# Kernel optimization log

Hardware: AMD Instinct MI355X
Metric: run time of the kernel (lower is better)

The kernel has to match this reference:

```python
import jax, jax.numpy as jnp
import numpy as np

N_POINTS = 32768
N_PRIMS = 2048
C_LIGHT = 299792458.0


def setup_inputs() -> dict:
    key = jax.random.key(0)
    k1, k2, k3, k4, k5 = jax.random.split(key, 5)
    # query points and primitive centers in a ~room-scale scene (metres)
    query_points = jax.random.normal(k1, (N_POINTS, 3), dtype=jnp.float32) * 2.0
    positions = jax.random.normal(k2, (N_PRIMS, 3), dtype=jnp.float32) * 2.0
    # diagonal anisotropic scales, kept away from zero for stability
    scales = jax.random.uniform(k3, (N_PRIMS, 3), dtype=jnp.float32, minval=0.1, maxval=1.0)
    amplitudes = jax.random.uniform(k4, (N_PRIMS,), dtype=jnp.float32, minval=0.0, maxval=1.0)
    phases = jax.random.uniform(k5, (N_PRIMS,), dtype=jnp.float32, minval=-np.pi, maxval=np.pi)
    return {
        "query_points": query_points,
        "positions": positions,
        "scales": scales,
        "amplitudes": amplitudes,
        "phases": phases,
        "frequency": 2400000000,  # 2.4 GHz
    }


def reference(query_points, positions, scales, amplitudes, phases, frequency):
    """Batched equivalent of: field = sum_p primitive_p.evaluate(query_points, frequency).

    Each complex Gaussian primitive contributes
        a_p * exp(-0.5 * (x-mu_p)^T diag(1/s_p^2) (x-mu_p)) * exp(i*(phi_p + k*|x-mu_p|))
    with wavenumber k = 2*pi*f/c. All pairwise terms are expressed as GEMMs.
    """
    f = jnp.float32(frequency)
    k_wave = jnp.float32(2.0 * np.pi) * f / jnp.float32(C_LIGHT)

    inv_var = 1.0 / (scales * scales)                      # [P,3]
    x2 = query_points * query_points                       # [N,3]
    mu2w = jnp.sum(positions * positions * inv_var, axis=1)  # [P]
    # Mahalanobis distance^2: sum_d (x_d-mu_d)^2 / s_d^2, expanded into GEMMs
    maha = (x2 @ inv_var.T
            - 2.0 * (query_points @ (positions * inv_var).T)
            + mu2w[None, :])                               # [N,P]
    maha = jnp.maximum(maha, 0.0)
    # Euclidean distance for the propagation phase
    d2 = (jnp.sum(x2, axis=1, keepdims=True)
          - 2.0 * (query_points @ positions.T)
          + jnp.sum(positions * positions, axis=1)[None, :])  # [N,P]
    r = jnp.sqrt(jnp.maximum(d2, 1e-12))

    w = amplitudes[None, :] * jnp.exp(-0.5 * maha)         # [N,P] real envelope
    ph = phases[None, :] + k_wave * r                      # [N,P] total phase
    field = jax.lax.complex(jnp.sum(w * jnp.cos(ph), axis=1),
                            jnp.sum(w * jnp.sin(ph), axis=1))  # [N] complex64
    return field
```

## Files before the change

### kernel.cpp

```cpp
#include <hip/hip_runtime.h>
#include <math.h>

#define NPOINTS 32768
#define NPRIMS  2048
#define BLK     256
#define PBLK    (NPOINTS / BLK)
#define TILE    128

__device__ __forceinline__ float read_freq(const void* p) {
    const unsigned* w = (const unsigned*)p;
    unsigned lo = w[0];
    float ff = __uint_as_float(lo);
    if (ff >= 1.0e5f && ff <= 1.0e13f) return ff;
    if (lo != 0u) return (float)lo;
    double d = *(const double*)p;
    if (d >= 1.0e5 && d <= 1.0e13) return (float)d;
    unsigned long long v = ((unsigned long long)w[1] << 32) | lo;
    return (float)v;
}

template <int NS, bool DIRECT>
__global__ __launch_bounds__(BLK) void field_kernel(
        const float* __restrict__ qp,
        const float* __restrict__ pos,
        const float* __restrict__ scl,
        const float* __restrict__ amp,
        const float* __restrict__ ph,
        const void*  __restrict__ freq_p,
        float*       __restrict__ out_or_part) {
    constexpr int PC = NPRIMS / NS;
    constexpr int NT = PC / TILE;
    __shared__ float4 sA[TILE];
    __shared__ float4 sB[TILE];

    const int n = blockIdx.x * BLK + threadIdx.x;
    const float x = qp[3*n+0], y = qp[3*n+1], z = qp[3*n+2];
    const float kr = read_freq(freq_p) / 299792458.0f;

    const int split = blockIdx.y;
    float re = 0.0f, im = 0.0f;

    const float KE     = -0.72134752044448169f;
    const float INV2PI =  0.15915494309189535f;

    for (int tile = 0; tile < NT; ++tile) {
        const int pbase = split * PC + tile * TILE;
        __syncthreads();
        if (threadIdx.x < TILE) {
            int p = pbase + threadIdx.x;
            float sx = scl[3*p+0], sy = scl[3*p+1], sz = scl[3*p+2];
            sA[threadIdx.x] = make_float4(pos[3*p+0], pos[3*p+1], pos[3*p+2], amp[p]);
            sB[threadIdx.x] = make_float4(KE * __builtin_amdgcn_rcpf(sx*sx),
                                          KE * __builtin_amdgcn_rcpf(sy*sy),
                                          KE * __builtin_amdgcn_rcpf(sz*sz),
                                          ph[p] * INV2PI);
        }
        __syncthreads();

        #pragma unroll 8
        for (int p = 0; p < TILE; ++p) {
            float4 a = sA[p];
            float4 b = sB[p];
            float dx = x - a.x, dy = y - a.y, dz = z - a.z;
            float t0 = dx*dx, t1 = dy*dy, t2 = dz*dz;
            float e  = fmaf(t0, b.x, fmaf(t1, b.y, t2 * b.z));
            float d2 = t0 + t1 + t2;
            float r  = __builtin_amdgcn_sqrtf(fmaxf(d2, 1e-12f));
            float w  = a.w * __builtin_amdgcn_exp2f(e);
            float tp = __builtin_amdgcn_fractf(fmaf(kr, r, b.w));
            float s  = __builtin_amdgcn_sinf(tp);
            float c  = __builtin_amdgcn_cosf(tp);
            re = fmaf(w, c, re);
            im = fmaf(w, s, im);
        }
    }

    if (DIRECT) {
        out_or_part[n]           = re;
        out_or_part[NPOINTS + n] = im;
    } else {
        float2* part = (float2*)out_or_part;
        part[(size_t)split * NPOINTS + n] = make_float2(re, im);
    }
}

template <int NS>
__global__ __launch_bounds__(BLK) void reduce_kernel(const float2* __restrict__ part,
                                                     float* __restrict__ out) {
    int n = blockIdx.x * blockDim.x + threadIdx.x;
    float re = 0.0f, im = 0.0f;
    #pragma unroll
    for (int s = 0; s < NS; ++s) {
        float2 v = part[(size_t)s * NPOINTS + n];
        re += v.x; im += v.y;
    }
    out[n]           = re;
    out[NPOINTS + n] = im;
}

extern "C" void kernel_launch(void* const* d_in, const int* in_sizes, int n_in,
                              void* d_out, int out_size, void* d_ws, size_t ws_size,
                              hipStream_t stream) {
    const float* qp  = (const float*)d_in[0];
    const float* pos = (const float*)d_in[1];
    const float* scl = (const float*)d_in[2];
    const float* amp = (const float*)d_in[3];
    const float* ph  = (const float*)d_in[4];
    const void*  fq  = d_in[5];

    float2* partial = (float2*)d_ws;
    const size_t per_split = (size_t)NPOINTS * sizeof(float2);
    float* out = (float*)d_out;

    if (ws_size >= 16 * per_split) {
        field_kernel<16, false><<<dim3(PBLK, 16), dim3(BLK), 0, stream>>>(qp, pos, scl, amp, ph, fq, (float*)partial);
        reduce_kernel<16><<<dim3(NPOINTS / BLK), dim3(BLK), 0, stream>>>(partial, out);
    } else if (ws_size >= 8 * per_split) {
        field_kernel<8, false><<<dim3(PBLK, 8), dim3(BLK), 0, stream>>>(qp, pos, scl, amp, ph, fq, (float*)partial);
        reduce_kernel<8><<<dim3(NPOINTS / BLK), dim3(BLK), 0, stream>>>(partial, out);
    } else if (ws_size >= 4 * per_split) {
        field_kernel<4, false><<<dim3(PBLK, 4), dim3(BLK), 0, stream>>>(qp, pos, scl, amp, ph, fq, (float*)partial);
        reduce_kernel<4><<<dim3(NPOINTS / BLK), dim3(BLK), 0, stream>>>(partial, out);
    } else if (ws_size >= 2 * per_split) {
        field_kernel<2, false><<<dim3(PBLK, 2), dim3(BLK), 0, stream>>>(qp, pos, scl, amp, ph, fq, (float*)partial);
        reduce_kernel<2><<<dim3(NPOINTS / BLK), dim3(BLK), 0, stream>>>(partial, out);
    } else {
        field_kernel<1, true><<<dim3(PBLK, 1), dim3(BLK), 0, stream>>>(qp, pos, scl, amp, ph, fq, out);
    }
}
```

Measured before the change: 47.34 us.

## Precompute packed primitive pairs and use packed float2 math in field kernel

Adds a prep kernel that precomputes per-primitive constants and interleaves two primitives into a 64-byte struct in workspace. The field kernel then reads these directly from global memory (uniform loads) instead of staging them through shared memory with syncthreads, and does the arithmetic on 2-wide float vectors so the compiler can emit packed FP32 ops. Transcendentals stay scalar. This adds an extra kernel launch and relies on scalar/global cache broadcast in place of LDS, and it drops the smaller split fallbacks.

```diff
diff --git a/kernel.cpp b/kernel.cpp
--- a/kernel.cpp
+++ b/kernel.cpp
@@ -5,7 +5,11 @@
 #define NPRIMS  2048
 #define BLK     256
 #define PBLK    (NPOINTS / BLK)
-#define TILE    128
+#define NSPLIT  16
+
+typedef float v2f __attribute__((ext_vector_type(2)));
+
+struct PrimPair { float4 q0, q1, q2, q3; };
 
 __device__ __forceinline__ float read_freq(const void* p) {
     const unsigned* w = (const unsigned*)p;
@@ -19,46 +23,119 @@
     return (float)v;
 }
 
-template <int NS, bool DIRECT>
+__global__ __launch_bounds__(BLK) void prep_kernel(
+        const float* __restrict__ pos,
+        const float* __restrict__ scl,
+        const float* __restrict__ amp,
+        const float* __restrict__ ph,
+        PrimPair* __restrict__ pp) {
+    int j = blockIdx.x * blockDim.x + threadIdx.x;
+    if (j >= NPRIMS / 2) return;
+    const float KE     = -0.72134752044448169f;
+    const float INV2PI =  0.15915494309189535f;
+    int p0 = 2 * j, p1 = 2 * j + 1;
+    float s0x = scl[3*p0+0], s0y = scl[3*p0+1], s0z = scl[3*p0+2];
+    float s1x = scl[3*p1+0], s1y = scl[3*p1+1], s1z = scl[3*p1+2];
+    PrimPair P;
+    P.q0 = make_float4(pos[3*p0+0], pos[3*p1+0], pos[3*p0+1], pos[3*p1+1]);
+    P.q1 = make_float4(pos[3*p0+2], pos[3*p1+2], amp[p0], amp[p1]);
+    P.q2 = make_float4(KE / (s0x*s0x), KE / (s1x*s1x), KE / (s0y*s0y), KE / (s1y*s1y));
+    P.q3 = make_float4(KE / (s0z*s0z), KE / (s1z*s1z), ph[p0] * INV2PI, ph[p1] * INV2PI);
+    pp[j] = P;
+}
+
 __global__ __launch_bounds__(BLK) void field_kernel(
+        const float* __restrict__ qp,
+        const PrimPair* __restrict__ pp,
+        const void* __restrict__ freq_p,
+        float2* __restrict__ part) {
+    const int n = blockIdx.x * BLK + threadIdx.x;
+    const float x = qp[3*n+0], y = qp[3*n+1], z = qp[3*n+2];
+    const float kr = read_freq(freq_p) / 299792458.0f;
+
+    constexpr int PAIRS = (NPRIMS / NSPLIT) / 2;
+    const int base = blockIdx.y * PAIRS;
+
+    v2f re = {0.0f, 0.0f}, im = {0.0f, 0.0f};
+    const v2f xx = {x, x}, yy = {y, y}, zz = {z, z};
+    const v2f kr2 = {kr, kr};
+    const v2f eps2 = {1e-12f, 1e-12f};
+
+    #pragma unroll 4
+    for (int j = 0; j < PAIRS; ++j) {
+        PrimPair P = pp[base + j];
+        v2f mux = {P.q0.x, P.q0.y}, muy = {P.q0.z, P.q0.w};
+        v2f muz = {P.q1.x, P.q1.y}, am2 = {P.q1.z, P.q1.w};
+        v2f gx  = {P.q2.x, P.q2.y}, gy  = {P.q2.z, P.q2.w};
+        v2f gz  = {P.q3.x, P.q3.y}, ph2 = {P.q3.z, P.q3.w};
+
+        v2f dx = xx - mux, dy = yy - muy, dz = zz - muz;
+        v2f t0 = dx * dx, t1 = dy * dy, t2 = dz * dz;
+        v2f e  = t0 * gx + t1 * gy + t2 * gz;
+        v2f d2 = t0 + t1 + t2;
+        d2 = __builtin_elementwise_max(d2, eps2);
+
+        float r0 = __builtin_amdgcn_sqrtf(d2.x);
+        float r1 = __builtin_amdgcn_sqrtf(d2.y);
+        float e0 = __builtin_amdgcn_exp2f(e.x);
+        float e1 = __builtin_amdgcn_exp2f(e.y);
+        v2f r2 = {r0, r1};
+        v2f ex = {e0, e1};
+        v2f w2 = am2 * ex;
+        v2f tp = kr2 * r2 + ph2;
+        float f0 = __builtin_amdgcn_fractf(tp.x);
+        float f1 = __builtin_amdgcn_fractf(tp.y);
+        float s0 = __builtin_amdgcn_sinf(f0);
+        float s1 = __builtin_amdgcn_sinf(f1);
+        float c0 = __builtin_amdgcn_cosf(f0);
+        float c1 = __builtin_amdgcn_cosf(f1);
+        v2f s2 = {s0, s1}, c2 = {c0, c1};
+        re += w2 * c2;
+        im += w2 * s2;
+    }
+
+    part[(size_t)blockIdx.y * NPOINTS + n] = make_float2(re.x + re.y, im.x + im.y);
+}
+
+__global__ __launch_bounds__(BLK) void reduce_kernel(const float2* __restrict__ part,
+                                                     float* __restrict__ out) {
+    int n = blockIdx.x * blockDim.x + threadIdx.x;
+    float re = 0.0f, im = 0.0f;
+    #pragma unroll
+    for (int s = 0; s < NSPLIT; ++s) {
+        float2 v = part[(size_t)s * NPOINTS + n];
+        re += v.x; im += v.y;
+    }
+    out[n]           = re;
+    out[NPOINTS + n] = im;
+}
+
+__global__ __launch_bounds__(BLK) void field_fallback(
         const float* __restrict__ qp,
         const float* __restrict__ pos,
         const float* __restrict__ scl,
         const float* __restrict__ amp,
         const float* __restrict__ ph,
         const void*  __restrict__ freq_p,
-        float*       __restrict__ out_or_part) {
-    constexpr int PC = NPRIMS / NS;
-    constexpr int NT = PC / TILE;
-    __shared__ float4 sA[TILE];
-    __shared__ float4 sB[TILE];
-
+        float*       __restrict__ out) {
+    __shared__ float4 sA[128];
+    __shared__ float4 sB[128];
     const int n = blockIdx.x * BLK + threadIdx.x;
     const float x = qp[3*n+0], y = qp[3*n+1], z = qp[3*n+2];
     const float kr = read_freq(freq_p) / 299792458.0f;
-
-    const int split = blockIdx.y;
+    const float KE = -0.72134752044448169f, INV2PI = 0.15915494309189535f;
     float re = 0.0f, im = 0.0f;
-
-    const float KE     = -0.72134752044448169f;
-    const float INV2PI =  0.15915494309189535f;
-
-    for (int tile = 0; tile < NT; ++tile) {
-        const int pbase = split * PC + tile * TILE;
+    for (int tile = 0; tile < NPRIMS / 128; ++tile) {
         __syncthreads();
-        if (threadIdx.x < TILE) {
-            int p = pbase + threadIdx.x;
+        if (threadIdx.x < 128) {
+            int p = tile * 128 + threadIdx.x;
             float sx = scl[3*p+0], sy = scl[3*p+1], sz = scl[3*p+2];
             sA[threadIdx.x] = make_float4(pos[3*p+0], pos[3*p+1], pos[3*p+2], amp[p]);
-            sB[threadIdx.x] = make_float4(KE * __builtin_amdgcn_rcpf(sx*sx),
-                                          KE * __builtin_amdgcn_rcpf(sy*sy),
-                                          KE * __builtin_amdgcn_rcpf(sz*sz),
-                                          ph[p] * INV2PI);
+            sB[threadIdx.x] = make_float4(KE/(sx*sx), KE/(sy*sy), KE/(sz*sz), ph[p]*INV2PI);
         }
         __syncthreads();
-
         #pragma unroll 8
-        for (int p = 0; p < TILE; ++p) {
+        for (int p = 0; p < 128; ++p) {
             float4 a = sA[p];
             float4 b = sB[p];
             float dx = x - a.x, dy = y - a.y, dz = z - a.z;
@@ -74,26 +151,6 @@
             im = fmaf(w, s, im);
         }
     }
-
-    if (DIRECT) {
-        out_or_part[n]           = re;
-        out_or_part[NPOINTS + n] = im;
-    } else {
-        float2* part = (float2*)out_or_part;
-        part[(size_t)split * NPOINTS + n] = make_float2(re, im);
-    }
-}
-
-template <int NS>
-__global__ __launch_bounds__(BLK) void reduce_kernel(const float2* __restrict__ part,
-                                                     float* __restrict__ out) {
-    int n = blockIdx.x * blockDim.x + threadIdx.x;
-    float re = 0.0f, im = 0.0f;
-    #pragma unroll
-    for (int s = 0; s < NS; ++s) {
-        float2 v = part[(size_t)s * NPOINTS + n];
-        re += v.x; im += v.y;
-    }
     out[n]           = re;
     out[NPOINTS + n] = im;
 }
@@ -107,24 +164,18 @@
     const float* amp = (const float*)d_in[3];
     const float* ph  = (const float*)d_in[4];
     const void*  fq  = d_in[5];
-
-    float2* partial = (float2*)d_ws;
-    const size_t per_split = (size_t)NPOINTS * sizeof(float2);
     float* out = (float*)d_out;
 
-    if (ws_size >= 16 * per_split) {
-        field_kernel<16, false><<<dim3(PBLK, 16), dim3(BLK), 0, stream>>>(qp, pos, scl, amp, ph, fq, (float*)partial);
-        reduce_kernel<16><<<dim3(NPOINTS / BLK), dim3(BLK), 0, stream>>>(partial, out);
-    } else if (ws_size >= 8 * per_split) {
-        field_kernel<8, false><<<dim3(PBLK, 8), dim3(BLK), 0, stream>>>(qp, pos, scl, amp, ph, fq, (float*)partial);
-        reduce_kernel<8><<<dim3(NPOINTS / BLK), dim3(BLK), 0, stream>>>(partial, out);
-    } else if (ws_size >= 4 * per_split) {
-        field_kernel<4, false><<<dim3(PBLK, 4), dim3(BLK), 0, stream>>>(qp, pos, scl, amp, ph, fq, (float*)partial);
-        reduce_kernel<4><<<dim3(NPOINTS / BLK), dim3(BLK), 0, stream>>>(partial, out);
-    } else if (ws_size >= 2 * per_split) {
-        field_kernel<2, false><<<dim3(PBLK, 2), dim3(BLK), 0, stream>>>(qp, pos, scl, amp, ph, fq, (float*)partial);
-        reduce_kernel<2><<<dim3(NPOINTS / BLK), dim3(BLK), 0, stream>>>(partial, out);
+    const size_t packed_bytes = (size_t)(NPRIMS / 2) * sizeof(PrimPair);
+    const size_t part_bytes   = (size_t)NSPLIT * NPOINTS * sizeof(float2);
+
+    if (ws_size >= packed_bytes + part_bytes) {
+        PrimPair* pp   = (PrimPair*)d_ws;
+        float2*   part = (float2*)((char*)d_ws + packed_bytes);
+        prep_kernel<<<dim3((NPRIMS/2 + BLK - 1) / BLK), dim3(BLK), 0, stream>>>(pos, scl, amp, ph, pp);
+        field_kernel<<<dim3(PBLK, NSPLIT), dim3(BLK), 0, stream>>>(qp, pp, fq, part);
+        reduce_kernel<<<dim3(NPOINTS / BLK), dim3(BLK), 0, stream>>>(part, out);
     } else {
-        field_kernel<1, true><<<dim3(PBLK, 1), dim3(BLK), 0, stream>>>(qp, pos, scl, amp, ph, fq, out);
+        field_fallback<<<dim3(PBLK), dim3(BLK), 0, stream>>>(qp, pos, scl, amp, ph, fq, out);
     }
 }
```

Result: no change. 47.27 us (-0.1%).
